# Performance work log

Hardware: AMD Instinct MI355X
Metric: run time of the kernel (lower is better)

The kernel has to match this reference:

```python
import jax, jax.numpy as jnp
import numpy as np

N = 100000      # nodes
E = 1600000     # edges (before self-loops)
F_IN = 128
H1, C1 = 8, 8   # layer 1: 8 heads x 8 channels
H2, C2 = 1, 64  # layer 2: 1 head x 64 channels
NEG_SLOPE = 0.2


def setup_inputs() -> dict:
    key = jax.random.key(0)
    ks = jax.random.split(key, 10)
    x = jax.random.normal(ks[0], (N, F_IN), jnp.float32)
    edge_index = jax.random.randint(ks[1], (2, E), 0, N, dtype=jnp.int32)
    s1 = 1.0 / np.sqrt(F_IN)
    s2 = 1.0 / np.sqrt(H1 * C1)
    return {
        "x": x,
        "edge_index": edge_index,
        "W1": jax.random.normal(ks[2], (F_IN, H1 * C1), jnp.float32) * s1,
        "a_src1": jax.random.normal(ks[3], (H1, C1), jnp.float32) * s1,
        "a_dst1": jax.random.normal(ks[4], (H1, C1), jnp.float32) * s1,
        "b1": jnp.zeros((H1 * C1,), jnp.float32),
        "W2": jax.random.normal(ks[5], (H1 * C1, H2 * C2), jnp.float32) * s2,
        "a_src2": jax.random.normal(ks[6], (H2, C2), jnp.float32) * s2,
        "a_dst2": jax.random.normal(ks[7], (H2, C2), jnp.float32) * s2,
        "b2": jnp.zeros((C2,), jnp.float32),
    }


def gat_conv(x, W, a_src, a_dst, b, src, dst, heads, out_ch, concat):
    """PyG-style GATConv (eval mode, self-loops already in src/dst)."""
    n = x.shape[0]
    h = (x @ W).reshape(n, heads, out_ch)            # [N, H, C]
    alpha_s = jnp.sum(h * a_src, axis=-1)            # [N, H]
    alpha_d = jnp.sum(h * a_dst, axis=-1)            # [N, H]
    e = alpha_s[src] + alpha_d[dst]                  # [E, H]
    e = jnp.where(e > 0, e, NEG_SLOPE * e)           # leaky relu
    # segment softmax grouped by destination node
    m = jax.ops.segment_max(e, dst, num_segments=n)  # [N, H]
    m = jnp.where(jnp.isfinite(m), m, 0.0)
    p = jnp.exp(e - m[dst])                          # [E, H]
    denom = jax.ops.segment_sum(p, dst, num_segments=n)
    alpha = p / (denom[dst] + 1e-16)                 # [E, H]
    # weighted scatter-add aggregation
    out = jax.ops.segment_sum(h[src] * alpha[:, :, None], dst, num_segments=n)
    out = out.reshape(n, heads * out_ch) if concat else out.mean(axis=1)
    return out + b


def reference(x, edge_index, W1, a_src1, a_dst1, b1, W2, a_src2, a_dst2, b2):
    n = x.shape[0]
    loops = jnp.arange(n, dtype=edge_index.dtype)    # PyG adds self-loops
    src = jnp.concatenate([edge_index[0], loops])
    dst = jnp.concatenate([edge_index[1], loops])
    h = gat_conv(x, W1, a_src1, a_dst1, b1, src, dst, H1, C1, True)
    h = jax.nn.elu(h)
    h = gat_conv(h, W2, a_src2, a_dst2, b2, src, dst, H2, C2, False)
    return jax.nn.log_softmax(h, axis=1)
```

## Files before the change

kernel.cpp:

```cpp
#include <hip/hip_runtime.h>
#include <math.h>

#define NEG_SLOPE 0.2f
#define CHUNK 4096
#define NPART 64
#define SLICECAP 128
#define CAP 48

typedef __attribute__((ext_vector_type(8))) short bf16x8;
typedef __attribute__((ext_vector_type(4))) float f32x4;

__device__ __forceinline__ unsigned short f2bf(float f) {
    unsigned int u = __float_as_uint(f);
    unsigned int r = (u + 0x7FFFu + ((u >> 16) & 1u)) >> 16;
    return (unsigned short)r;
}
__device__ __forceinline__ float bfl(unsigned int u) { return __uint_as_float(u << 16); }
__device__ __forceinline__ float bfh(unsigned int u) { return __uint_as_float(u & 0xffff0000u); }

__global__ void bucket_slice(const int* __restrict__ ei, int E, int nchunks, int PR,
                             int2* __restrict__ qds, int* __restrict__ scnt) {
    __shared__ int lcnt[8][NPART];
    __shared__ int lbase[8][NPART];
    int tid = threadIdx.x, wave = tid >> 6;
    int chunk = blockIdx.x;
    int base = chunk * CHUNK;
    for (int i = tid; i < 8 * NPART; i += 512) ((int*)lcnt)[i] = 0;
    __syncthreads();
    int d[8], s[8], b[8], pos[8];
    #pragma unroll
    for (int k = 0; k < 8; ++k) {
        int t = base + k * 512 + tid;
        bool v = t < E;
        d[k] = v ? ei[E + t] : 0;
        s[k] = v ? ei[t] : 0;
        b[k] = v ? (d[k] / PR) : -1;
    }
    #pragma unroll
    for (int k = 0; k < 8; ++k)
        pos[k] = (b[k] >= 0) ? atomicAdd(&lcnt[wave][b[k]], 1) : 0;
    __syncthreads();
    if (tid < NPART) {
        int run = 0;
        #pragma unroll
        for (int w = 0; w < 8; ++w) { lbase[w][tid] = run; run += lcnt[w][tid]; }
        scnt[tid * nchunks + chunk] = run;
    }
    __syncthreads();
    #pragma unroll
    for (int k = 0; k < 8; ++k) {
        if (b[k] >= 0) {
            int p = lbase[wave][b[k]] + pos[k];
            if (p < SLICECAP)
                qds[(size_t)(b[k] * nchunks + chunk) * SLICECAP + p] = make_int2(d[k], s[k]);
        }
    }
}

__global__ void scatter_lds(const int2* __restrict__ qds, const int* __restrict__ scnt,
                            int nchunks, int PR, int N,
                            int* __restrict__ cnt, int* __restrict__ col) {
    extern __shared__ int lc[];
    int b = blockIdx.x;
    int lo = b * PR;
    int tid = threadIdx.x, lane = tid & 63, wave = tid >> 6;
    int nwaves = blockDim.x >> 6;
    for (int i = tid; i < PR; i += blockDim.x) lc[i] = 0;
    __syncthreads();
    for (int sl = wave; sl < nchunks; sl += nwaves) {
        int n = min(scnt[b * nchunks + sl], SLICECAP);
        const int2* q = qds + (size_t)(b * nchunks + sl) * SLICECAP;
        for (int i = lane; i < n; i += 64) {
            int2 e = q[i];
            int p = atomicAdd(&lc[e.x - lo], 1);
            if (p < CAP - 1)
                col[e.x * CAP + p] = e.y;
        }
    }
    __syncthreads();
    for (int i = tid; i < PR; i += blockDim.x) {
        int d = lo + i;
        if (d < N) {
            int p = min(lc[i], CAP - 1);
            col[d * CAP + p] = d;
            cnt[d] = p + 1;
        }
    }
}

template<int K, int H, typename AT>
__global__ __launch_bounds__(256) void gemm_mfma(const AT* __restrict__ A,
                                                 const float* __restrict__ W,
                                                 unsigned short* __restrict__ Hb,
                                                 const float* __restrict__ a_src,
                                                 const float* __restrict__ a_dst,
                                                 float* __restrict__ AS,
                                                 float* __restrict__ AD, int N) {
    constexpr int LD = K + 8;
    __shared__ __align__(16) unsigned short Wt[64 * LD];
    __shared__ __align__(16) unsigned short Xl[64 * LD];
    const int tid = threadIdx.x;
    const int lane = tid & 63, wave = tid >> 6;
    const int l16 = lane & 15, q = lane >> 4;
    const int lcol = (lane & 3) * 16;
    for (int i = tid; i < K * 64; i += 256) {
        int k = i >> 6, c = i & 63;
        Wt[c * LD + k] = f2bf(W[i]);
    }
    float4 asv0 = *(const float4*)&a_src[lcol];
    float4 asv1 = *(const float4*)&a_src[lcol + 4];
    float4 asv2 = *(const float4*)&a_src[lcol + 8];
    float4 asv3 = *(const float4*)&a_src[lcol + 12];
    float4 adv0 = *(const float4*)&a_dst[lcol];
    float4 adv1 = *(const float4*)&a_dst[lcol + 4];
    float4 adv2 = *(const float4*)&a_dst[lcol + 8];
    float4 adv3 = *(const float4*)&a_dst[lcol + 12];
    __syncthreads();
    for (int rb = blockIdx.x; rb * 64 < N; rb += gridDim.x) {
        int r0 = rb * 64;
        if (sizeof(AT) == 4) {
            const float* Af = (const float*)A;
            for (int i = tid; i < 64 * (K / 4); i += 256) {
                int row = i / (K / 4), kq = i % (K / 4);
                int rg = min(r0 + row, N - 1);
                float4 a = *(const float4*)&Af[(size_t)rg * K + kq * 4];
                unsigned short* p = &Xl[row * LD + kq * 4];
                p[0] = f2bf(a.x); p[1] = f2bf(a.y); p[2] = f2bf(a.z); p[3] = f2bf(a.w);
            }
        } else {
            const unsigned short* Ab = (const unsigned short*)A;
            for (int i = tid; i < 64 * (K / 8); i += 256) {
                int row = i / (K / 8), k8 = i % (K / 8);
                int rg = min(r0 + row, N - 1);
                uint4 a = *(const uint4*)&Ab[(size_t)rg * K + k8 * 8];
                *(uint4*)&Xl[row * LD + k8 * 8] = a;
            }
        }
        __syncthreads();
        f32x4 acc[4] = {{0.f,0.f,0.f,0.f},{0.f,0.f,0.f,0.f},{0.f,0.f,0.f,0.f},{0.f,0.f,0.f,0.f}};
        #pragma unroll
        for (int kk = 0; kk < K / 32; ++kk) {
            bf16x8 af = *(bf16x8*)&Xl[(wave * 16 + l16) * LD + kk * 32 + q * 8];
            #pragma unroll
            for (int c = 0; c < 4; ++c) {
                bf16x8 bfr = *(bf16x8*)&Wt[(c * 16 + l16) * LD + kk * 32 + q * 8];
                acc[c] = __builtin_amdgcn_mfma_f32_16x16x32_bf16(af, bfr, acc[c], 0, 0, 0);
            }
        }
        #pragma unroll
        for (int c = 0; c < 4; ++c)
            #pragma unroll
            for (int r = 0; r < 4; ++r)
                Xl[(wave * 16 + q * 4 + r) * LD + c * 16 + l16] = f2bf(acc[c][r]);
        int lrow = wave * 16 + (lane >> 2);
        int node = r0 + lrow;
        uint4 o0 = *(uint4*)&Xl[lrow * LD + lcol];
        uint4 o1 = *(uint4*)&Xl[lrow * LD + lcol + 8];
        if (node < N) {
            *(uint4*)&Hb[(size_t)node * 64 + lcol] = o0;
            *(uint4*)&Hb[(size_t)node * 64 + lcol + 8] = o1;
            float sl = bfl(o0.x)*asv0.x + bfh(o0.x)*asv0.y + bfl(o0.y)*asv0.z + bfh(o0.y)*asv0.w
                     + bfl(o0.z)*asv1.x + bfh(o0.z)*asv1.y + bfl(o0.w)*asv1.z + bfh(o0.w)*asv1.w;
            float sh = bfl(o1.x)*asv2.x + bfh(o1.x)*asv2.y + bfl(o1.y)*asv2.z + bfh(o1.y)*asv2.w
                     + bfl(o1.z)*asv3.x + bfh(o1.z)*asv3.y + bfl(o1.w)*asv3.z + bfh(o1.w)*asv3.w;
            float dl = bfl(o0.x)*adv0.x + bfh(o0.x)*adv0.y + bfl(o0.y)*adv0.z + bfh(o0.y)*adv0.w
                     + bfl(o0.z)*adv1.x + bfh(o0.z)*adv1.y + bfl(o0.w)*adv1.z + bfh(o0.w)*adv1.w;
            float dh = bfl(o1.x)*adv2.x + bfh(o1.x)*adv2.y + bfl(o1.y)*adv2.z + bfh(o1.y)*adv2.w
                     + bfl(o1.z)*adv3.x + bfh(o1.z)*adv3.y + bfl(o1.w)*adv3.z + bfh(o1.w)*adv3.w;
            if (H == 8) {
                float2 sv = {sl, sh};
                float2 dv = {dl, dh};
                *(float2*)&AS[(size_t)node * 8 + (lane & 3) * 2] = sv;
                *(float2*)&AD[(size_t)node * 8 + (lane & 3) * 2] = dv;
            } else {
                float s = sl + sh, d = dl + dh;
                s += __shfl_xor(s, 1, 64); s += __shfl_xor(s, 2, 64);
                d += __shfl_xor(d, 1, 64); d += __shfl_xor(d, 2, 64);
                if ((lane & 3) == 0) { AS[node] = s; AD[node] = d; }
            }
        }
        __syncthreads();
    }
}

template<int H, bool FINAL>
__global__ __launch_bounds__(256, 4) void aggregate(
                          const int* __restrict__ cnt, const int* __restrict__ col,
                          const float* __restrict__ AS, const float* __restrict__ AD,
                          const uint4* __restrict__ Hb, const float* __restrict__ bias,
                          void* __restrict__ OUT, int N) {
    int lane = threadIdx.x & 63;
    int wid = (blockIdx.x * blockDim.x + threadIdx.x) >> 6;
    int nw = (gridDim.x * blockDim.x) >> 6;
    int slot = lane >> 3, l8 = lane & 7;
    const int h = (H == 8) ? l8 : 0;
    float4 b4a = *(const float4*)&bias[l8 * 8];
    float4 b4b = *(const float4*)&bias[l8 * 8 + 4];
    for (int nb0 = wid * 8; nb0 < N; nb0 += nw * 8) {
        int n = nb0 + slot;
        bool nok = n < N;
        int nc = nok ? n : (N - 1);
        int beg = nc * CAP;
        int deg = cnt[nc];
        float ad = AD[(size_t)nc * H + h];
        int maxd = deg;
        #pragma unroll
        for (int off = 8; off <= 32; off <<= 1)
            maxd = max(maxd, __shfl_xor(maxd, off, 64));
        float den = 0.0f;
        float acc[8] = {0.f, 0.f, 0.f, 0.f, 0.f, 0.f, 0.f, 0.f};
        int myc = (l8 < deg) ? col[beg + l8] : -1;
        for (int j0 = 0; j0 < maxd; j0 += 8) {
            int mnext = (j0 + 8 + l8 < deg) ? col[beg + j0 + 8 + l8] : -1;
            int sarr[8];
            #pragma unroll
            for (int jj = 0; jj < 8; ++jj)
                sarr[jj] = __shfl(myc, slot * 8 + jj, 64);
            float ev[8];
            uint4 hvv[8];
            #pragma unroll
            for (int jj = 0; jj < 8; ++jj) {
                if (sarr[jj] >= 0) {
                    ev[jj]  = AS[(size_t)sarr[jj] * H + h];
                    hvv[jj] = Hb[(size_t)sarr[jj] * 8 + l8];
                }
            }
            #pragma unroll
            for (int jj = 0; jj < 8; ++jj) {
                if (sarr[jj] >= 0) {
                    float e = ev[jj] + ad;
                    e = e > 0.0f ? e : NEG_SLOPE * e;
                    float p = __expf(e);
                    den += p;
                    uint4 hv = hvv[jj];
                    acc[0] = fmaf(p, bfl(hv.x), acc[0]);
                    acc[1] = fmaf(p, bfh(hv.x), acc[1]);
                    acc[2] = fmaf(p, bfl(hv.y), acc[2]);
                    acc[3] = fmaf(p, bfh(hv.y), acc[3]);
                    acc[4] = fmaf(p, bfl(hv.z), acc[4]);
                    acc[5] = fmaf(p, bfh(hv.z), acc[5]);
                    acc[6] = fmaf(p, bfl(hv.w), acc[6]);
                    acc[7] = fmaf(p, bfh(hv.w), acc[7]);
                }
            }
            myc = mnext;
        }
        float inv = 1.0f / (den + 1e-16f);
        float v[8];
        v[0] = acc[0] * inv + b4a.x; v[1] = acc[1] * inv + b4a.y;
        v[2] = acc[2] * inv + b4a.z; v[3] = acc[3] * inv + b4a.w;
        v[4] = acc[4] * inv + b4b.x; v[5] = acc[5] * inv + b4b.y;
        v[6] = acc[6] * inv + b4b.z; v[7] = acc[7] * inv + b4b.w;
        if (!FINAL) {
            #pragma unroll
            for (int i = 0; i < 8; ++i) v[i] = v[i] > 0.0f ? v[i] : __expf(v[i]) - 1.0f;
            if (nok) {
                union { unsigned short u[8]; uint4 q; } pk;
                #pragma unroll
                for (int i = 0; i < 8; ++i) pk.u[i] = f2bf(v[i]);
                ((uint4*)OUT)[(size_t)n * 8 + l8] = pk.q;
            }
        } else {
            float m = v[0];
            #pragma unroll
            for (int i = 1; i < 8; ++i) m = fmaxf(m, v[i]);
            #pragma unroll
            for (int off = 1; off <= 4; off <<= 1) m = fmaxf(m, __shfl_xor(m, off, 64));
            float ss = 0.0f;
            #pragma unroll
            for (int i = 0; i < 8; ++i) ss += __expf(v[i] - m);
            #pragma unroll
            for (int off = 1; off <= 4; off <<= 1) ss += __shfl_xor(ss, off, 64);
            float lse = m + __logf(ss);
            if (nok) {
                float* Of = (float*)OUT;
                float4 o0 = {v[0] - lse, v[1] - lse, v[2] - lse, v[3] - lse};
                float4 o1 = {v[4] - lse, v[5] - lse, v[6] - lse, v[7] - lse};
                *(float4*)&Of[(size_t)n * 64 + l8 * 8] = o0;
                *(float4*)&Of[(size_t)n * 64 + l8 * 8 + 4] = o1;
            }
        }
    }
}

extern "C" void kernel_launch(void* const* d_in, const int* in_sizes, int n_in,
                              void* d_out, int out_size, void* d_ws, size_t ws_size,
                              hipStream_t stream) {
    const float* x    = (const float*)d_in[0];
    const int*   ei   = (const int*)d_in[1];
    const float* W1   = (const float*)d_in[2];
    const float* as1w = (const float*)d_in[3];
    const float* ad1w = (const float*)d_in[4];
    const float* b1   = (const float*)d_in[5];
    const float* W2   = (const float*)d_in[6];
    const float* as2w = (const float*)d_in[7];
    const float* ad2w = (const float*)d_in[8];
    const float* b2   = (const float*)d_in[9];
    const int N = in_sizes[0] / 128;
    const int E = in_sizes[1] / 2;
    const int nchunks = (E + CHUNK - 1) / CHUNK;
    const int PR = (N + NPART - 1) / NPART;

    float* ws = (float*)d_ws;
    size_t off = 0;
    unsigned short* AGG1b = (unsigned short*)(ws + off); off += (size_t)N * 32;
    unsigned short* h1b   = (unsigned short*)(ws + off); off += (size_t)N * 32;
    unsigned short* h2b   = (unsigned short*)(ws + off); off += (size_t)N * 32;
    int2* qds = (int2*)ws;
    float* AS1  = ws + off; off += (size_t)N * 8;
    float* AD1  = ws + off; off += (size_t)N * 8;
    float* AS2  = ws + off; off += N;
    float* AD2  = ws + off; off += N;
    int* cnt    = (int*)(ws + off);
    int* scnt   = cnt + N;
    int* col    = scnt + NPART * nchunks;

    bucket_slice<<<nchunks, 512, 0, stream>>>(ei, E, nchunks, PR, qds, scnt);
    scatter_lds<<<NPART, 1024, PR * sizeof(int), stream>>>(qds, scnt, nchunks,
                                                           PR, N, cnt, col);

    gemm_mfma<128, 8, float><<<1563, 256, 0, stream>>>(x, W1, h1b, as1w, ad1w,
                                                       AS1, AD1, N);
    aggregate<8, false><<<3125, 256, 0, stream>>>(cnt, col, AS1, AD1,
                                                  (const uint4*)h1b, b1, AGG1b, N);
    gemm_mfma<64, 1, unsigned short><<<1563, 256, 0, stream>>>(AGG1b, W2, h2b,
                                                               as2w, ad2w, AS2, AD2, N);
    aggregate<1, true><<<3125, 256, 0, stream>>>(cnt, col, AS2, AD2,
                                                 (const uint4*)h2b, b2, d_out, N);
}
```

Before: 265.2 us.

## Replace two-pass bucketed adjacency build with single global-atomic pass

Replaces the bucket_slice + scatter_lds two-kernel CSR build, which staged edges through partition slices and LDS atomics, with a memset plus one kernel that does global atomicAdd per edge, self-loops included, into fixed-capacity rows. It also packs bf16 conversions into one 64-bit LDS store in the GEMM and halves the aggregate grid size. Global atomics on a random destination array can contend, and the self-loop no longer has a reserved slot, so a node at capacity could drop its self-loop. Edge order within a row becomes nondeterministic.

```diff
diff --git a/kernel.cpp b/kernel.cpp
--- a/kernel.cpp
+++ b/kernel.cpp
@@ -2,9 +2,6 @@
 #include <math.h>
 
 #define NEG_SLOPE 0.2f
-#define CHUNK 4096
-#define NPART 64
-#define SLICECAP 128
 #define CAP 48
 
 typedef __attribute__((ext_vector_type(8))) short bf16x8;
@@ -18,73 +15,19 @@
 __device__ __forceinline__ float bfl(unsigned int u) { return __uint_as_float(u << 16); }
 __device__ __forceinline__ float bfh(unsigned int u) { return __uint_as_float(u & 0xffff0000u); }
 
-__global__ void bucket_slice(const int* __restrict__ ei, int E, int nchunks, int PR,
-                             int2* __restrict__ qds, int* __restrict__ scnt) {
-    __shared__ int lcnt[8][NPART];
-    __shared__ int lbase[8][NPART];
-    int tid = threadIdx.x, wave = tid >> 6;
-    int chunk = blockIdx.x;
-    int base = chunk * CHUNK;
-    for (int i = tid; i < 8 * NPART; i += 512) ((int*)lcnt)[i] = 0;
-    __syncthreads();
-    int d[8], s[8], b[8], pos[8];
-    #pragma unroll
-    for (int k = 0; k < 8; ++k) {
-        int t = base + k * 512 + tid;
-        bool v = t < E;
-        d[k] = v ? ei[E + t] : 0;
-        s[k] = v ? ei[t] : 0;
-        b[k] = v ? (d[k] / PR) : -1;
-    }
-    #pragma unroll
-    for (int k = 0; k < 8; ++k)
-        pos[k] = (b[k] >= 0) ? atomicAdd(&lcnt[wave][b[k]], 1) : 0;
-    __syncthreads();
-    if (tid < NPART) {
-        int run = 0;
-        #pragma unroll
-        for (int w = 0; w < 8; ++w) { lbase[w][tid] = run; run += lcnt[w][tid]; }
-        scnt[tid * nchunks + chunk] = run;
-    }
-    __syncthreads();
-    #pragma unroll
-    for (int k = 0; k < 8; ++k) {
-        if (b[k] >= 0) {
-            int p = lbase[wave][b[k]] + pos[k];
-            if (p < SLICECAP)
-                qds[(size_t)(b[k] * nchunks + chunk) * SLICECAP + p] = make_int2(d[k], s[k]);
-        }
-    }
-}
-
-__global__ void scatter_lds(const int2* __restrict__ qds, const int* __restrict__ scnt,
-                            int nchunks, int PR, int N,
-                            int* __restrict__ cnt, int* __restrict__ col) {
-    extern __shared__ int lc[];
-    int b = blockIdx.x;
-    int lo = b * PR;
-    int tid = threadIdx.x, lane = tid & 63, wave = tid >> 6;
-    int nwaves = blockDim.x >> 6;
-    for (int i = tid; i < PR; i += blockDim.x) lc[i] = 0;
-    __syncthreads();
-    for (int sl = wave; sl < nchunks; sl += nwaves) {
-        int n = min(scnt[b * nchunks + sl], SLICECAP);
-        const int2* q = qds + (size_t)(b * nchunks + sl) * SLICECAP;
-        for (int i = lane; i < n; i += 64) {
-            int2 e = q[i];
-            int p = atomicAdd(&lc[e.x - lo], 1);
-            if (p < CAP - 1)
-                col[e.x * CAP + p] = e.y;
-        }
-    }
-    __syncthreads();
-    for (int i = tid; i < PR; i += blockDim.x) {
-        int d = lo + i;
-        if (d < N) {
-            int p = min(lc[i], CAP - 1);
-            col[d * CAP + p] = d;
-            cnt[d] = p + 1;
-        }
+__global__ __launch_bounds__(256) void build_adj(const int* __restrict__ ei,
+                                                 int E, int N,
+                                                 int* __restrict__ cnt,
+                                                 int* __restrict__ col) {
+    int total = E + N;
+    for (int t = blockIdx.x * blockDim.x + threadIdx.x; t < total;
+         t += gridDim.x * blockDim.x) {
+        int s, d;
+        if (t < E) { s = ei[t]; d = ei[E + t]; }
+        else       { s = t - E; d = t - E; }
+        int p = atomicAdd(&cnt[d], 1);
+        if (p < CAP)
+            col[d * CAP + p] = s;
     }
 }
 
@@ -124,8 +67,9 @@
                 int row = i / (K / 4), kq = i % (K / 4);
                 int rg = min(r0 + row, N - 1);
                 float4 a = *(const float4*)&Af[(size_t)rg * K + kq * 4];
-                unsigned short* p = &Xl[row * LD + kq * 4];
-                p[0] = f2bf(a.x); p[1] = f2bf(a.y); p[2] = f2bf(a.z); p[3] = f2bf(a.w);
+                unsigned int u0 = (unsigned int)f2bf(a.x) | ((unsigned int)f2bf(a.y) << 16);
+                unsigned int u1 = (unsigned int)f2bf(a.z) | ((unsigned int)f2bf(a.w) << 16);
+                *(uint2*)&Xl[row * LD + kq * 4] = make_uint2(u0, u1);
             }
         } else {
             const unsigned short* Ab = (const unsigned short*)A;
@@ -201,7 +145,7 @@
         bool nok = n < N;
         int nc = nok ? n : (N - 1);
         int beg = nc * CAP;
-        int deg = cnt[nc];
+        int deg = min(cnt[nc], CAP);
         float ad = AD[(size_t)nc * H + h];
         int maxd = deg;
         #pragma unroll
@@ -298,33 +242,28 @@
     const float* b2   = (const float*)d_in[9];
     const int N = in_sizes[0] / 128;
     const int E = in_sizes[1] / 2;
-    const int nchunks = (E + CHUNK - 1) / CHUNK;
-    const int PR = (N + NPART - 1) / NPART;
 
     float* ws = (float*)d_ws;
     size_t off = 0;
     unsigned short* AGG1b = (unsigned short*)(ws + off); off += (size_t)N * 32;
     unsigned short* h1b   = (unsigned short*)(ws + off); off += (size_t)N * 32;
     unsigned short* h2b   = (unsigned short*)(ws + off); off += (size_t)N * 32;
-    int2* qds = (int2*)ws;
     float* AS1  = ws + off; off += (size_t)N * 8;
     float* AD1  = ws + off; off += (size_t)N * 8;
     float* AS2  = ws + off; off += N;
     float* AD2  = ws + off; off += N;
     int* cnt    = (int*)(ws + off);
-    int* scnt   = cnt + N;
-    int* col    = scnt + NPART * nchunks;
-
-    bucket_slice<<<nchunks, 512, 0, stream>>>(ei, E, nchunks, PR, qds, scnt);
-    scatter_lds<<<NPART, 1024, PR * sizeof(int), stream>>>(qds, scnt, nchunks,
-                                                           PR, N, cnt, col);
+    int* col    = cnt + N;
+
+    hipMemsetAsync(cnt, 0, N * sizeof(int), stream);
+    build_adj<<<2048, 256, 0, stream>>>(ei, E, N, cnt, col);
 
     gemm_mfma<128, 8, float><<<1563, 256, 0, stream>>>(x, W1, h1b, as1w, ad1w,
                                                        AS1, AD1, N);
-    aggregate<8, false><<<3125, 256, 0, stream>>>(cnt, col, AS1, AD1,
+    aggregate<8, false><<<1563, 256, 0, stream>>>(cnt, col, AS1, AD1,
                                                   (const uint4*)h1b, b1, AGG1b, N);
     gemm_mfma<64, 1, unsigned short><<<1563, 256, 0, stream>>>(AGG1b, W2, h2b,
                                                                as2w, ad2w, AS2, AD2, N);
-    aggregate<1, true><<<3125, 256, 0, stream>>>(cnt, col, AS2, AD2,
+    aggregate<1, true><<<1563, 256, 0, stream>>>(cnt, col, AS2, AD2,
                                                  (const uint4*)h2b, b2, d_out, N);
 }
```

Result: slower. 356.3 us (+34.3%).
